# Performance work log

Hardware: AMD Instinct MI355X
Metric: run time of the kernel (lower is better)

## Reference

```python
import jax, jax.numpy as jnp
import numpy as np

MODEL_D = 512
N_HEADS = 8
D_K = 64
D_V = 64
EPS = 1e-5


def _layer_norm(x, g, b):
    mu = jnp.mean(x, axis=-1, keepdims=True)
    var = jnp.mean((x - mu) ** 2, axis=-1, keepdims=True)
    return (x - mu) * jax.lax.rsqrt(var + EPS) * g + b


def setup_inputs() -> dict:
    key = jax.random.key(0)
    ks = jax.random.split(key, 8)
    B, S = 8, 1024
    smiles = jax.random.normal(ks[0], (B, S, MODEL_D), dtype=jnp.float32)
    # causal mask: True where attention is disallowed (masked_fill semantics)
    mask = jnp.broadcast_to(jnp.triu(jnp.ones((S, S), dtype=bool), k=1), (B, S, S))
    sd = 1.0 / np.sqrt(MODEL_D)
    w_q = jax.random.normal(ks[1], (MODEL_D, N_HEADS * D_K), dtype=jnp.float32) * sd
    w_k = jax.random.normal(ks[2], (MODEL_D, N_HEADS * D_K), dtype=jnp.float32) * sd
    w_v = jax.random.normal(ks[3], (MODEL_D, N_HEADS * D_V), dtype=jnp.float32) * sd
    w_o = jax.random.normal(ks[4], (N_HEADS * D_V, MODEL_D), dtype=jnp.float32) * sd
    w1 = jax.random.normal(ks[5], (MODEL_D, 4 * MODEL_D), dtype=jnp.float32) * sd
    w2 = jax.random.normal(ks[6], (4 * MODEL_D, MODEL_D), dtype=jnp.float32) * (1.0 / np.sqrt(4 * MODEL_D))
    ln1_g = jnp.ones((MODEL_D,), jnp.float32)
    ln1_b = jnp.zeros((MODEL_D,), jnp.float32)
    ln2_g = jnp.ones((MODEL_D,), jnp.float32)
    ln2_b = jnp.zeros((MODEL_D,), jnp.float32)
    return {"smiles": smiles, "mask": mask, "w_q": w_q, "w_k": w_k, "w_v": w_v,
            "w_o": w_o, "ln1_g": ln1_g, "ln1_b": ln1_b, "w1": w1, "w2": w2,
            "ln2_g": ln2_g, "ln2_b": ln2_b}


def reference(smiles, mask, w_q, w_k, w_v, w_o, ln1_g, ln1_b, w1, w2, ln2_g, ln2_b):
    B, S, _ = smiles.shape
    # QKV projections -> [B, H, S, d]
    q = (smiles @ w_q).reshape(B, S, N_HEADS, D_K).transpose(0, 2, 1, 3)
    k = (smiles @ w_k).reshape(B, S, N_HEADS, D_K).transpose(0, 2, 1, 3)
    v = (smiles @ w_v).reshape(B, S, N_HEADS, D_V).transpose(0, 2, 1, 3)
    scores = jnp.einsum("bhqd,bhkd->bhqk", q, k) / np.sqrt(D_K)
    scores = jnp.where(mask[:, None, :, :], jnp.float32(-1e9), scores)
    attention = jax.nn.softmax(scores, axis=-1)
    ctx = jnp.einsum("bhqk,bhkd->bhqd", attention, v)
    ctx = ctx.transpose(0, 2, 1, 3).reshape(B, S, N_HEADS * D_V)
    attn_out = _layer_norm(ctx @ w_o + smiles, ln1_g, ln1_b)
    ffn = jax.nn.relu(attn_out @ w1) @ w2
    out = _layer_norm(ffn + attn_out, ln2_g, ln2_b)
    return out, attention
```

## Files before the change

kernel.cpp:

```cpp
#include <hip/hip_runtime.h>
#include <math.h>

#define BATCH 8
#define SEQ   1024
#define DMODEL 512
#define NHEADS 8
#define DKV   64
#define DFF   2048
#define ROWS  (BATCH * SEQ)
#define QKLD  1536

typedef __attribute__((ext_vector_type(8))) short short8;
typedef __attribute__((ext_vector_type(4))) float f32x4;

__device__ __forceinline__ short f2bf(float f) {
    unsigned u = __float_as_uint(f);
    u += 0x7FFFu + ((u >> 16) & 1u);
    return (short)(u >> 16);
}
__device__ __forceinline__ float bf2f(short s) {
    return __uint_as_float(((unsigned)(unsigned short)s) << 16);
}

#define GLD16(g, l) __builtin_amdgcn_global_load_lds( \
    (const __attribute__((address_space(1))) void*)(g), \
    (__attribute__((address_space(3))) void*)(l), 16, 0, 0)

__device__ __forceinline__ void stage128x32(const short* __restrict__ g, int ld,
                                            short* lds, int tid) {
    const int w = tid >> 6;
#pragma unroll
    for (int i = 0; i < 2; ++i) {
        const int L = i * 256 + tid;
        const int r = L >> 2, c = (L & 3) << 3;
        GLD16(g + (size_t)r * ld + c, lds + (size_t)(i * 256 + (w << 6)) * 8);
    }
}

template<int OUT_BF16, int RELU>
__global__ __launch_bounds__(256) void gemm_bt(const short* __restrict__ A,
                                               const short* __restrict__ Bt,
                                               void* __restrict__ Cv,
                                               int K, int lda, int ldb, int ldc,
                                               int qcols) {
    __shared__ short As[2][128 * 32];
    __shared__ short Bs[2][128 * 32];
    const int tid = threadIdx.x;

    const int nx = gridDim.x;
    const int nwg = nx * gridDim.y;
    const int flat = blockIdx.y * nx + blockIdx.x;
    const int swz = (flat & 7) * (nwg >> 3) + (flat >> 3);
    const int m0 = (swz / nx) * 128, n0 = (swz % nx) * 128;

    const int w = tid >> 6, lane = tid & 63;
    const int wr = (w >> 1) * 64, wc = (w & 1) * 64;
    const int lrow = lane & 15, hi = lane >> 4;

    f32x4 acc[4][4];
#pragma unroll
    for (int m = 0; m < 4; ++m)
#pragma unroll
        for (int n = 0; n < 4; ++n) acc[m][n] = {0.f, 0.f, 0.f, 0.f};

    const short* Ab = A + (size_t)m0 * lda;
    const short* Bb = Bt + (size_t)n0 * ldb;
    const int nt = K >> 5;

    stage128x32(Ab, lda, As[0], tid);
    stage128x32(Bb, ldb, Bs[0], tid);
    __syncthreads();

    int cur = 0;
    for (int t = 0; t < nt; ++t) {
        if (t + 1 < nt) {
            stage128x32(Ab + (size_t)(t + 1) * 32, lda, As[cur ^ 1], tid);
            stage128x32(Bb + (size_t)(t + 1) * 32, ldb, Bs[cur ^ 1], tid);
        }

        short8 af[4], bfr[4];
#pragma unroll
        for (int m = 0; m < 4; ++m)
            af[m] = *(const short8*)&As[cur][(size_t)(wr + m * 16 + lrow) * 32 + hi * 8];
#pragma unroll
        for (int n = 0; n < 4; ++n)
            bfr[n] = *(const short8*)&Bs[cur][(size_t)(wc + n * 16 + lrow) * 32 + hi * 8];
#pragma unroll
        for (int m = 0; m < 4; ++m)
#pragma unroll
            for (int n = 0; n < 4; ++n)
                acc[m][n] = __builtin_amdgcn_mfma_f32_16x16x32_bf16(bfr[n], af[m], acc[m][n], 0, 0, 0);

        __syncthreads();
        cur ^= 1;
    }

    const int orow = m0 + wr + lrow;
    const int ocol0 = n0 + wc + hi * 4;
#pragma unroll
    for (int m = 0; m < 4; ++m)
#pragma unroll
        for (int n = 0; n < 4; ++n) {
            const int col = ocol0 + n * 16;
            const float cs = (col < qcols) ? 0.125f : 1.0f;
            float v0 = acc[m][n][0], v1 = acc[m][n][1], v2 = acc[m][n][2], v3 = acc[m][n][3];
            if (RELU) {
                v0 = fmaxf(v0, 0.f); v1 = fmaxf(v1, 0.f);
                v2 = fmaxf(v2, 0.f); v3 = fmaxf(v3, 0.f);
            }
            v0 *= cs; v1 *= cs; v2 *= cs; v3 *= cs;
            const size_t off = (size_t)(orow + m * 16) * ldc + col;
            if (OUT_BF16) {
                short4 st = { f2bf(v0), f2bf(v1), f2bf(v2), f2bf(v3) };
                *(short4*)((short*)Cv + off) = st;
            } else {
                float4 st = { v0, v1, v2, v3 };
                *(float4*)((float*)Cv + off) = st;
            }
        }
}

__global__ __launch_bounds__(256, 2) void fused_attn(const short* __restrict__ Q,
                                                     const short* __restrict__ K,
                                                     const short* __restrict__ Vt,
                                                     float* __restrict__ attnP,
                                                     short* __restrict__ ctx) {
    const int flat = blockIdx.y * 8 + blockIdx.x;
    const int swz  = (flat & 7) * 64 + (flat >> 3);
    const int bh = swz >> 3, it = 7 - (swz & 7);
    const int b = bh >> 3, h = bh & 7;

    __shared__ short Qs[128 * 64];
    __shared__ short KVs[2][128 * 64];
    __shared__ short Ps[128 * 128];
    float* rsum = (float*)Ps;

    const int tid = threadIdx.x;
    const int w = tid >> 6, lane = tid & 63;
    const int wr = (w >> 1) * 64, wc2 = (w & 1);
    const int lrow = lane & 15, hi = lane >> 4;
    const size_t base = (size_t)b * SEQ * QKLD + h * DKV;
    float* aprow = attnP + (size_t)bh * SEQ * SEQ;

    auto stage_k = [&](int kt, short* dst) {
#pragma unroll
        for (int i = 0; i < 4; ++i) {
            const int L = i * 256 + tid;
            const int r = L >> 3, sc = ((L & 7) ^ (r & 7)) * 8;
            GLD16(K + base + (size_t)(kt * 128 + r) * QKLD + sc,
                  dst + (size_t)(i * 256 + (w << 6)) * 8);
        }
    };
    auto stage_v = [&](int kt, short* dst) {
#pragma unroll
        for (int i = 0; i < 4; ++i) {
            const int L = i * 256 + tid;
            const int r = L >> 4, sc = ((L & 15) ^ (r & 7)) * 8;
            GLD16(Vt + (size_t)(bh * DKV + r) * SEQ + kt * 128 + sc,
                  dst + (size_t)(i * 256 + (w << 6)) * 8);
        }
    };
    auto qkt = [&](const short* Ks, f32x4 s[4][4]) {
#pragma unroll
        for (int m = 0; m < 4; ++m)
#pragma unroll
            for (int n = 0; n < 4; ++n) s[m][n] = {0.f, 0.f, 0.f, 0.f};
#pragma unroll
        for (int sk = 0; sk < 2; ++sk) {
            short8 qf[4], kf[4];
#pragma unroll
            for (int m = 0; m < 4; ++m) {
                const int r = wr + m * 16 + lrow;
                qf[m] = *(const short8*)((const char*)Qs + r * 128 + ((hi * 16 + sk * 64) ^ ((r & 7) << 4)));
            }
#pragma unroll
            for (int n = 0; n < 4; ++n) {
                const int r = wc2 * 64 + n * 16 + lrow;
                kf[n] = *(const short8*)((const char*)Ks + r * 128 + ((hi * 16 + sk * 64) ^ ((r & 7) << 4)));
            }
#pragma unroll
            for (int m = 0; m < 4; ++m)
#pragma unroll
                for (int n = 0; n < 4; ++n)
                    s[m][n] = __builtin_amdgcn_mfma_f32_16x16x32_bf16(kf[n], qf[m], s[m][n], 0, 0, 0);
        }
    };

    {
        const int nz4 = (7 - it) * 32;
        if (nz4 > 0) {
            for (int r = tid >> 5; r < 128; r += 8) {
                float4* rp = (float4*)(aprow + (size_t)(it * 128 + r) * SEQ + (it + 1) * 128);
                for (int c = tid & 31; c < nz4; c += 32)
                    rp[c] = make_float4(0.f, 0.f, 0.f, 0.f);
            }
        }
    }

#pragma unroll
    for (int i = 0; i < 4; ++i) {
        const int L = i * 256 + tid;
        const int r = L >> 3, sc = ((L & 7) ^ (r & 7)) * 8;
        GLD16(Q + base + (size_t)(it * 128 + r) * QKLD + sc,
              Qs + (size_t)(i * 256 + (w << 6)) * 8);
    }
    stage_k(0, KVs[0]);
    stage_v(0, KVs[1]);
    __syncthreads();

    float rs[4] = {0.f, 0.f, 0.f, 0.f};
    f32x4 o[4][2];
#pragma unroll
    for (int m = 0; m < 4; ++m)
#pragma unroll
        for (int n = 0; n < 2; ++n) o[m][n] = {0.f, 0.f, 0.f, 0.f};

    for (int kt = 0; kt <= it; ++kt) {
        f32x4 s[4][4];
        qkt(KVs[0], s);

        const bool diag = (kt == it);
#pragma unroll
        for (int m = 0; m < 4; ++m) {
            const int q = wr + m * 16 + lrow;
#pragma unroll
            for (int n = 0; n < 4; ++n) {
                const int k0 = wc2 * 64 + n * 16 + hi * 4;
                float p0 = __expf(s[m][n][0]);
                float p1 = __expf(s[m][n][1]);
                float p2 = __expf(s[m][n][2]);
                float p3 = __expf(s[m][n][3]);
                if (diag) {
                    if (k0 + 0 > q) p0 = 0.f;
                    if (k0 + 1 > q) p1 = 0.f;
                    if (k0 + 2 > q) p2 = 0.f;
                    if (k0 + 3 > q) p3 = 0.f;
                }
                rs[m] += (p0 + p1) + (p2 + p3);
                short4 ph = { f2bf(p0), f2bf(p1), f2bf(p2), f2bf(p3) };
                *(short4*)((char*)Ps + q * 256 + ((k0 * 2) ^ ((q & 7) << 4))) = ph;
            }
        }
        __syncthreads();
        if (kt < it) stage_k(kt + 1, KVs[0]);

#pragma unroll
        for (int sk = 0; sk < 4; ++sk) {
            short8 pf[4], vf[2];
#pragma unroll
            for (int m = 0; m < 4; ++m) {
                const int r = wr + m * 16 + lrow;
                pf[m] = *(const short8*)((const char*)Ps + r * 256 + ((hi * 16 + sk * 64) ^ ((r & 7) << 4)));
            }
#pragma unroll
            for (int n = 0; n < 2; ++n) {
                const int r = wc2 * 32 + n * 16 + lrow;
                vf[n] = *(const short8*)((const char*)KVs[1] + r * 256 + ((hi * 16 + sk * 64) ^ ((r & 7) << 4)));
            }
#pragma unroll
            for (int m = 0; m < 4; ++m)
#pragma unroll
                for (int n = 0; n < 2; ++n)
                    o[m][n] = __builtin_amdgcn_mfma_f32_16x16x32_bf16(vf[n], pf[m], o[m][n], 0, 0, 0);
        }
        __syncthreads();
        if (kt < it) stage_v(kt + 1, KVs[1]);
    }

#pragma unroll
    for (int m = 0; m < 4; ++m) {
        rs[m] += __shfl_xor(rs[m], 16);
        rs[m] += __shfl_xor(rs[m], 32);
    }
    if (lane < 16) {
#pragma unroll
        for (int m = 0; m < 4; ++m)
            rsum[wc2 * 128 + wr + m * 16 + lane] = rs[m];
    }
    __syncthreads();
    if (tid < 128) rsum[tid] = 1.0f / (rsum[tid] + rsum[128 + tid]);
    __syncthreads();
    float inv[4];
#pragma unroll
    for (int m = 0; m < 4; ++m) inv[m] = rsum[wr + m * 16 + lrow];

#pragma unroll
    for (int m = 0; m < 4; ++m) {
        const int q = it * 128 + wr + m * 16 + lrow;
#pragma unroll
        for (int n = 0; n < 2; ++n) {
            const int d = h * DKV + wc2 * 32 + n * 16 + hi * 4;
            short4 st = { f2bf(o[m][n][0] * inv[m]), f2bf(o[m][n][1] * inv[m]),
                          f2bf(o[m][n][2] * inv[m]), f2bf(o[m][n][3] * inv[m]) };
            *(short4*)(ctx + (size_t)(b * SEQ + q) * DMODEL + d) = st;
        }
    }

    stage_k(0, KVs[0]);
    __syncthreads();
    int cur = 0;
    for (int kt = 0; kt <= it; ++kt) {
        if (kt < it) stage_k(kt + 1, KVs[cur ^ 1]);

        f32x4 s[4][4];
        qkt(KVs[cur], s);

        const bool diag = (kt == it);
#pragma unroll
        for (int m = 0; m < 4; ++m) {
            const int q = wr + m * 16 + lrow;
#pragma unroll
            for (int n = 0; n < 4; ++n) {
                const int k0 = wc2 * 64 + n * 16 + hi * 4;
                float p0 = __expf(s[m][n][0]);
                float p1 = __expf(s[m][n][1]);
                float p2 = __expf(s[m][n][2]);
                float p3 = __expf(s[m][n][3]);
                if (diag) {
                    if (k0 + 0 > q) p0 = 0.f;
                    if (k0 + 1 > q) p1 = 0.f;
                    if (k0 + 2 > q) p2 = 0.f;
                    if (k0 + 3 > q) p3 = 0.f;
                }
                float4 pv4 = { p0 * inv[m], p1 * inv[m], p2 * inv[m], p3 * inv[m] };
                *(float4*)(aprow + (size_t)(it * 128 + q) * SEQ + kt * 128 + k0) = pv4;
            }
        }
        __syncthreads();
        cur ^= 1;
    }
}

template<int RES_BF16, int OUT_F32, int OUT_BF16>
__global__ __launch_bounds__(128) void residual_ln(const float* __restrict__ xin,
                                                   const void* __restrict__ res,
                                                   const float* __restrict__ g,
                                                   const float* __restrict__ beta,
                                                   float* __restrict__ outf,
                                                   short* __restrict__ outh) {
    const int row = blockIdx.x;
    const int tid = threadIdx.x;

    float4 v = ((const float4*)(xin + (size_t)row * DMODEL))[tid];
    if (RES_BF16) {
        const short4 rr = ((const short4*)((const short*)res + (size_t)row * DMODEL))[tid];
        v.x += bf2f(rr.x); v.y += bf2f(rr.y); v.z += bf2f(rr.z); v.w += bf2f(rr.w);
    } else {
        const float4 rr = ((const float4*)((const float*)res + (size_t)row * DMODEL))[tid];
        v.x += rr.x; v.y += rr.y; v.z += rr.z; v.w += rr.w;
    }

    float sum = v.x + v.y + v.z + v.w;
    float sq  = v.x * v.x + v.y * v.y + v.z * v.z + v.w * v.w;
#pragma unroll
    for (int off = 32; off > 0; off >>= 1) {
        sum += __shfl_down(sum, off);
        sq  += __shfl_down(sq, off);
    }
    __shared__ float s_sum[2], s_sq[2];
    const int wid = tid >> 6, lane = tid & 63;
    if (lane == 0) { s_sum[wid] = sum; s_sq[wid] = sq; }
    __syncthreads();

    const float tsum = s_sum[0] + s_sum[1];
    const float tsq  = s_sq[0] + s_sq[1];
    const float mu   = tsum * (1.0f / DMODEL);
    const float var  = tsq * (1.0f / DMODEL) - mu * mu;
    const float rstd = rsqrtf(var + 1e-5f);

    const float4 gg = ((const float4*)g)[tid];
    const float4 bb = ((const float4*)beta)[tid];
    float4 o;
    o.x = (v.x - mu) * rstd * gg.x + bb.x;
    o.y = (v.y - mu) * rstd * gg.y + bb.y;
    o.z = (v.z - mu) * rstd * gg.z + bb.z;
    o.w = (v.w - mu) * rstd * gg.w + bb.w;
    if (OUT_F32) ((float4*)(outf + (size_t)row * DMODEL))[tid] = o;
    if (OUT_BF16) {
        short4 oh = { f2bf(o.x), f2bf(o.y), f2bf(o.z), f2bf(o.w) };
        ((short4*)(outh + (size_t)row * DMODEL))[tid] = oh;
    }
}

__global__ __launch_bounds__(256) void convert_bf16(const float* __restrict__ X,
                                                    short* __restrict__ Xh) {
    const size_t i = (size_t)blockIdx.x * 256 + threadIdx.x;
    const float4* p = (const float4*)X + i * 2;
    const float4 a = p[0], b = p[1];
    short8 o = { f2bf(a.x), f2bf(a.y), f2bf(a.z), f2bf(a.w),
                 f2bf(b.x), f2bf(b.y), f2bf(b.z), f2bf(b.w) };
    *(short8*)(Xh + i * 8) = o;
}

__global__ __launch_bounds__(256) void transpose_w(const float* __restrict__ W,
                                                   short* __restrict__ Wt,
                                                   int K, int N) {
    __shared__ float t[32][33];
    const int n0 = blockIdx.x * 32, k0 = blockIdx.y * 32;
    const int tx = threadIdx.x, ty = threadIdx.y;
#pragma unroll
    for (int i = 0; i < 4; ++i)
        t[ty + i * 8][tx] = W[(size_t)(k0 + ty + i * 8) * N + n0 + tx];
    __syncthreads();
#pragma unroll
    for (int i = 0; i < 4; ++i)
        Wt[(size_t)(n0 + ty + i * 8) * K + k0 + tx] = f2bf(t[tx][ty + i * 8]);
}

__global__ __launch_bounds__(256) void transpose_v(const short* __restrict__ QKV,
                                                   short* __restrict__ Vt) {
    __shared__ short t[32][33];
    const int s0 = blockIdx.x * 32, d0 = blockIdx.y * 32, bh = blockIdx.z;
    const int b = bh >> 3, h = bh & 7;
    const int tx = threadIdx.x, ty = threadIdx.y;
#pragma unroll
    for (int i = 0; i < 4; ++i)
        t[ty + i * 8][tx] = QKV[(size_t)(b * SEQ + s0 + ty + i * 8) * QKLD + 1024 + h * DKV + d0 + tx];
    __syncthreads();
#pragma unroll
    for (int i = 0; i < 4; ++i)
        Vt[(size_t)(bh * DKV + d0 + ty + i * 8) * SEQ + s0 + tx] = t[tx][ty + i * 8];
}

extern "C" void kernel_launch(void* const* d_in, const int* in_sizes, int n_in,
                              void* d_out, int out_size, void* d_ws, size_t ws_size,
                              hipStream_t stream) {
    const float* X    = (const float*)d_in[0];
    const float* w_q  = (const float*)d_in[2];
    const float* w_k  = (const float*)d_in[3];
    const float* w_v  = (const float*)d_in[4];
    const float* w_o  = (const float*)d_in[5];
    const float* ln1g = (const float*)d_in[6];
    const float* ln1b = (const float*)d_in[7];
    const float* w1   = (const float*)d_in[8];
    const float* w2   = (const float*)d_in[9];
    const float* ln2g = (const float*)d_in[10];
    const float* ln2b = (const float*)d_in[11];

    float* out   = (float*)d_out;
    float* attnP = out + (size_t)ROWS * DMODEL;

    const size_t M = 1u << 20;
    short* ws    = (short*)d_ws;
    short* qkv   = ws;
    short* Vt    = ws + 12 * M;
    short* ctxh  = ws + 16 * M;
    short* aoutH = ws + 20 * M;
    short* Xh    = ws + 24 * M;
    short* wqkvt = ws + 28 * M;
    short* wot   = wqkvt + 786432;
    short* w1t   = ws + 29 * M;
    short* w2t   = ws + 30 * M;
    short* hbuf  = ws;

    convert_bf16<<<dim3(2048), dim3(256), 0, stream>>>(X, Xh);
    transpose_w<<<dim3(16, 16), dim3(32, 8), 0, stream>>>(w_q, wqkvt, DMODEL, DMODEL);
    transpose_w<<<dim3(16, 16), dim3(32, 8), 0, stream>>>(w_k, wqkvt + 512 * 512, DMODEL, DMODEL);
    transpose_w<<<dim3(16, 16), dim3(32, 8), 0, stream>>>(w_v, wqkvt + 1024 * 512, DMODEL, DMODEL);
    transpose_w<<<dim3(16, 16), dim3(32, 8), 0, stream>>>(w_o, wot, DMODEL, DMODEL);
    transpose_w<<<dim3(64, 16), dim3(32, 8), 0, stream>>>(w1, w1t, DMODEL, DFF);
    transpose_w<<<dim3(16, 64), dim3(32, 8), 0, stream>>>(w2, w2t, DFF, DMODEL);

    gemm_bt<1, 0><<<dim3(12, 64), dim3(256), 0, stream>>>(Xh, wqkvt, qkv,
                                                          DMODEL, DMODEL, DMODEL, QKLD, 512);
    transpose_v<<<dim3(32, 2, 64), dim3(32, 8), 0, stream>>>(qkv, Vt);

    fused_attn<<<dim3(8, 64), dim3(256), 0, stream>>>(qkv, qkv + 512, Vt, attnP, ctxh);

    gemm_bt<0, 0><<<dim3(4, 64), dim3(256), 0, stream>>>(ctxh, wot, out,
                                                         DMODEL, DMODEL, DMODEL, DMODEL, 0);
    residual_ln<0, 0, 1><<<dim3(ROWS), dim3(128), 0, stream>>>(out, X, ln1g, ln1b, nullptr, aoutH);

    gemm_bt<1, 1><<<dim3(16, 64), dim3(256), 0, stream>>>(aoutH, w1t, hbuf,
                                                          DMODEL, DMODEL, DMODEL, DFF, 0);
    gemm_bt<0, 0><<<dim3(4, 64), dim3(256), 0, stream>>>(hbuf, w2t, out,
                                                         DFF, DFF, DFF, DMODEL, 0);
    residual_ln<1, 1, 0><<<dim3(ROWS), dim3(128), 0, stream>>>(out, aoutH, ln2g, ln2b, out, nullptr);
}
```

Measured before the change: 234.9 us.

## Defer attention-probability writes into FFN1 kernel and merge weight-prep launches

The attention kernel no longer recomputes QK^T to write the full probability matrix. It now stores the per-row inverse softmax sums to a small buffer. A new combined kernel interleaves FFN1 GEMM blocks with blocks that recompute scores and write the normalized probabilities and causal zeros, so the write-bandwidth-heavy output overlaps with compute-bound GEMM work. The input conversion and the six weight-transpose launches are also merged into one prep kernel, and workspace offsets are reshuffled to fit the new buffers. The cost is that the combined kernel uses a larger shared-memory footprint for all its blocks, and its heterogeneous blocks may balance unevenly.

```diff
diff --git a/kernel.cpp b/kernel.cpp
--- a/kernel.cpp
+++ b/kernel.cpp
@@ -34,6 +34,45 @@
         const int L = i * 256 + tid;
         const int r = L >> 2, c = (L & 3) << 3;
         GLD16(g + (size_t)r * ld + c, lds + (size_t)(i * 256 + (w << 6)) * 8);
+    }
+}
+
+__device__ __forceinline__ void stage_k128(const short* __restrict__ Kp, size_t base,
+                                           int kt, short* dst, int tid, int w) {
+#pragma unroll
+    for (int i = 0; i < 4; ++i) {
+        const int L = i * 256 + tid;
+        const int r = L >> 3, sc = ((L & 7) ^ (r & 7)) * 8;
+        GLD16(Kp + base + (size_t)(kt * 128 + r) * QKLD + sc,
+              dst + (size_t)(i * 256 + (w << 6)) * 8);
+    }
+}
+
+__device__ __forceinline__ void qkt_body(const short* Qs, const short* Ks,
+                                         int wr, int wc2, int lrow, int hi,
+                                         f32x4 s[4][4]) {
+#pragma unroll
+    for (int m = 0; m < 4; ++m)
+#pragma unroll
+        for (int n = 0; n < 4; ++n) s[m][n] = {0.f, 0.f, 0.f, 0.f};
+#pragma unroll
+    for (int sk = 0; sk < 2; ++sk) {
+        short8 qf[4], kf[4];
+#pragma unroll
+        for (int m = 0; m < 4; ++m) {
+            const int r = wr + m * 16 + lrow;
+            qf[m] = *(const short8*)((const char*)Qs + r * 128 + ((hi * 16 + sk * 64) ^ ((r & 7) << 4)));
+        }
+#pragma unroll
+        for (int n = 0; n < 4; ++n) {
+            const int r = wc2 * 64 + n * 16 + lrow;
+            kf[n] = *(const short8*)((const char*)Ks + r * 128 + ((hi * 16 + sk * 64) ^ ((r & 7) << 4)));
+        }
+#pragma unroll
+        for (int m = 0; m < 4; ++m)
+#pragma unroll
+            for (int n = 0; n < 4; ++n)
+                s[m][n] = __builtin_amdgcn_mfma_f32_16x16x32_bf16(kf[n], qf[m], s[m][n], 0, 0, 0);
     }
 }
 
@@ -77,7 +116,6 @@
             stage128x32(Ab + (size_t)(t + 1) * 32, lda, As[cur ^ 1], tid);
             stage128x32(Bb + (size_t)(t + 1) * 32, ldb, Bs[cur ^ 1], tid);
         }
-
         short8 af[4], bfr[4];
 #pragma unroll
         for (int m = 0; m < 4; ++m)
@@ -90,7 +128,6 @@
 #pragma unroll
             for (int n = 0; n < 4; ++n)
                 acc[m][n] = __builtin_amdgcn_mfma_f32_16x16x32_bf16(bfr[n], af[m], acc[m][n], 0, 0, 0);
-
         __syncthreads();
         cur ^= 1;
     }
@@ -120,11 +157,11 @@
         }
 }
 
-__global__ __launch_bounds__(256, 2) void fused_attn(const short* __restrict__ Q,
-                                                     const short* __restrict__ K,
-                                                     const short* __restrict__ Vt,
-                                                     float* __restrict__ attnP,
-                                                     short* __restrict__ ctx) {
+__global__ __launch_bounds__(256, 2) void attn_ctx(const short* __restrict__ Q,
+                                                   const short* __restrict__ K,
+                                                   const short* __restrict__ Vt,
+                                                   short* __restrict__ ctx,
+                                                   float* __restrict__ invg) {
     const int flat = blockIdx.y * 8 + blockIdx.x;
     const int swz  = (flat & 7) * 64 + (flat >> 3);
     const int bh = swz >> 3, it = 7 - (swz & 7);
@@ -140,17 +177,7 @@
     const int wr = (w >> 1) * 64, wc2 = (w & 1);
     const int lrow = lane & 15, hi = lane >> 4;
     const size_t base = (size_t)b * SEQ * QKLD + h * DKV;
-    float* aprow = attnP + (size_t)bh * SEQ * SEQ;
-
-    auto stage_k = [&](int kt, short* dst) {
-#pragma unroll
-        for (int i = 0; i < 4; ++i) {
-            const int L = i * 256 + tid;
-            const int r = L >> 3, sc = ((L & 7) ^ (r & 7)) * 8;
-            GLD16(K + base + (size_t)(kt * 128 + r) * QKLD + sc,
-                  dst + (size_t)(i * 256 + (w << 6)) * 8);
-        }
-    };
+
     auto stage_v = [&](int kt, short* dst) {
 #pragma unroll
         for (int i = 0; i < 4; ++i) {
@@ -160,42 +187,6 @@
                   dst + (size_t)(i * 256 + (w << 6)) * 8);
         }
     };
-    auto qkt = [&](const short* Ks, f32x4 s[4][4]) {
-#pragma unroll
-        for (int m = 0; m < 4; ++m)
-#pragma unroll
-            for (int n = 0; n < 4; ++n) s[m][n] = {0.f, 0.f, 0.f, 0.f};
-#pragma unroll
-        for (int sk = 0; sk < 2; ++sk) {
-            short8 qf[4], kf[4];
-#pragma unroll
-            for (int m = 0; m < 4; ++m) {
-                const int r = wr + m * 16 + lrow;
-                qf[m] = *(const short8*)((const char*)Qs + r * 128 + ((hi * 16 + sk * 64) ^ ((r & 7) << 4)));
-            }
-#pragma unroll
-            for (int n = 0; n < 4; ++n) {
-                const int r = wc2 * 64 + n * 16 + lrow;
-                kf[n] = *(const short8*)((const char*)Ks + r * 128 + ((hi * 16 + sk * 64) ^ ((r & 7) << 4)));
-            }
-#pragma unroll
-            for (int m = 0; m < 4; ++m)
-#pragma unroll
-                for (int n = 0; n < 4; ++n)
-                    s[m][n] = __builtin_amdgcn_mfma_f32_16x16x32_bf16(kf[n], qf[m], s[m][n], 0, 0, 0);
-        }
-    };
-
-    {
-        const int nz4 = (7 - it) * 32;
-        if (nz4 > 0) {
-            for (int r = tid >> 5; r < 128; r += 8) {
-                float4* rp = (float4*)(aprow + (size_t)(it * 128 + r) * SEQ + (it + 1) * 128);
-                for (int c = tid & 31; c < nz4; c += 32)
-                    rp[c] = make_float4(0.f, 0.f, 0.f, 0.f);
-            }
-        }
-    }
 
 #pragma unroll
     for (int i = 0; i < 4; ++i) {
@@ -204,7 +195,7 @@
         GLD16(Q + base + (size_t)(it * 128 + r) * QKLD + sc,
               Qs + (size_t)(i * 256 + (w << 6)) * 8);
     }
-    stage_k(0, KVs[0]);
+    stage_k128(K, base, 0, KVs[0], tid, w);
     stage_v(0, KVs[1]);
     __syncthreads();
 
@@ -217,7 +208,7 @@
 
     for (int kt = 0; kt <= it; ++kt) {
         f32x4 s[4][4];
-        qkt(KVs[0], s);
+        qkt_body(Qs, KVs[0], wr, wc2, lrow, hi, s);
 
         const bool diag = (kt == it);
 #pragma unroll
@@ -242,7 +233,7 @@
             }
         }
         __syncthreads();
-        if (kt < it) stage_k(kt + 1, KVs[0]);
+        if (kt < it) stage_k128(K, base, kt + 1, KVs[0], tid, w);
 
 #pragma unroll
         for (int sk = 0; sk < 4; ++sk) {
@@ -278,7 +269,11 @@
             rsum[wc2 * 128 + wr + m * 16 + lane] = rs[m];
     }
     __syncthreads();
-    if (tid < 128) rsum[tid] = 1.0f / (rsum[tid] + rsum[128 + tid]);
+    if (tid < 128) {
+        const float iv = 1.0f / (rsum[tid] + rsum[128 + tid]);
+        rsum[tid] = iv;
+        invg[(size_t)bh * SEQ + it * 128 + tid] = iv;
+    }
     __syncthreads();
     float inv[4];
 #pragma unroll
@@ -295,39 +290,148 @@
             *(short4*)(ctx + (size_t)(b * SEQ + q) * DMODEL + d) = st;
         }
     }
-
-    stage_k(0, KVs[0]);
-    __syncthreads();
-    int cur = 0;
-    for (int kt = 0; kt <= it; ++kt) {
-        if (kt < it) stage_k(kt + 1, KVs[cur ^ 1]);
-
-        f32x4 s[4][4];
-        qkt(KVs[cur], s);
-
-        const bool diag = (kt == it);
-#pragma unroll
-        for (int m = 0; m < 4; ++m) {
-            const int q = wr + m * 16 + lrow;
+}
+
+__global__ __launch_bounds__(256) void ffn1_pwrite(const short* __restrict__ Am,
+                                                   const short* __restrict__ w1t,
+                                                   short* __restrict__ hbuf,
+                                                   const short* __restrict__ Q,
+                                                   const short* __restrict__ K,
+                                                   const float* __restrict__ invg,
+                                                   float* __restrict__ attnP) {
+    __shared__ short smem[24576];
+    const int tid = threadIdx.x;
+    const int w = tid >> 6, lane = tid & 63;
+    const int lrow = lane & 15, hi = lane >> 4;
+    const int flat = blockIdx.x;
+
+    if (flat % 3 != 0) {
+        const int f = flat - flat / 3 - 1;
+        const int swz = (f & 7) * 128 + (f >> 3);
+        const int m0 = (swz >> 4) * 128, n0 = (swz & 15) * 128;
+        const int wr = (w >> 1) * 64, wc = (w & 1) * 64;
+
+        short* As0 = smem;
+        short* As1 = smem + 4096;
+        short* Bs0 = smem + 8192;
+        short* Bs1 = smem + 12288;
+
+        f32x4 acc[4][4];
+#pragma unroll
+        for (int m = 0; m < 4; ++m)
+#pragma unroll
+            for (int n = 0; n < 4; ++n) acc[m][n] = {0.f, 0.f, 0.f, 0.f};
+
+        const short* Ab = Am + (size_t)m0 * DMODEL;
+        const short* Bb = w1t + (size_t)n0 * DMODEL;
+
+        stage128x32(Ab, DMODEL, As0, tid);
+        stage128x32(Bb, DMODEL, Bs0, tid);
+        __syncthreads();
+
+        for (int t = 0; t < 16; ++t) {
+            short* Ac = (t & 1) ? As1 : As0;
+            short* Bc = (t & 1) ? Bs1 : Bs0;
+            if (t + 1 < 16) {
+                short* An = (t & 1) ? As0 : As1;
+                short* Bn = (t & 1) ? Bs0 : Bs1;
+                stage128x32(Ab + (size_t)(t + 1) * 32, DMODEL, An, tid);
+                stage128x32(Bb + (size_t)(t + 1) * 32, DMODEL, Bn, tid);
+            }
+            short8 af[4], bfr[4];
+#pragma unroll
+            for (int m = 0; m < 4; ++m)
+                af[m] = *(const short8*)&Ac[(size_t)(wr + m * 16 + lrow) * 32 + hi * 8];
+#pragma unroll
+            for (int n = 0; n < 4; ++n)
+                bfr[n] = *(const short8*)&Bc[(size_t)(wc + n * 16 + lrow) * 32 + hi * 8];
+#pragma unroll
+            for (int m = 0; m < 4; ++m)
+#pragma unroll
+                for (int n = 0; n < 4; ++n)
+                    acc[m][n] = __builtin_amdgcn_mfma_f32_16x16x32_bf16(bfr[n], af[m], acc[m][n], 0, 0, 0);
+            __syncthreads();
+        }
+
+        const int orow = m0 + wr + lrow;
+        const int ocol0 = n0 + wc + hi * 4;
+#pragma unroll
+        for (int m = 0; m < 4; ++m)
 #pragma unroll
             for (int n = 0; n < 4; ++n) {
-                const int k0 = wc2 * 64 + n * 16 + hi * 4;
-                float p0 = __expf(s[m][n][0]);
-                float p1 = __expf(s[m][n][1]);
-                float p2 = __expf(s[m][n][2]);
-                float p3 = __expf(s[m][n][3]);
-                if (diag) {
-                    if (k0 + 0 > q) p0 = 0.f;
-                    if (k0 + 1 > q) p1 = 0.f;
-                    if (k0 + 2 > q) p2 = 0.f;
-                    if (k0 + 3 > q) p3 = 0.f;
+                short4 st = { f2bf(fmaxf(acc[m][n][0], 0.f)), f2bf(fmaxf(acc[m][n][1], 0.f)),
+                              f2bf(fmaxf(acc[m][n][2], 0.f)), f2bf(fmaxf(acc[m][n][3], 0.f)) };
+                *(short4*)(hbuf + (size_t)(orow + m * 16) * DFF + ocol0 + n * 16) = st;
+            }
+    } else {
+        const int p = flat / 3;
+        const int swz = (p & 7) * 64 + (p >> 3);
+        const int bh = swz >> 3, it = 7 - (swz & 7);
+        const int b = bh >> 3, h = bh & 7;
+        const int wr = (w >> 1) * 64, wc2 = (w & 1);
+        const size_t base = (size_t)b * SEQ * QKLD + h * DKV;
+        float* aprow = attnP + (size_t)bh * SEQ * SEQ;
+
+        short* Qs  = smem;
+        short* Ks0 = smem + 8192;
+        short* Ks1 = smem + 16384;
+
+        {
+            const int nz4 = (7 - it) * 32;
+            if (nz4 > 0) {
+                for (int r = tid >> 5; r < 128; r += 8) {
+                    float4* rp = (float4*)(aprow + (size_t)(it * 128 + r) * SEQ + (it + 1) * 128);
+                    for (int c = tid & 31; c < nz4; c += 32)
+                        rp[c] = make_float4(0.f, 0.f, 0.f, 0.f);
                 }
-                float4 pv4 = { p0 * inv[m], p1 * inv[m], p2 * inv[m], p3 * inv[m] };
-                *(float4*)(aprow + (size_t)(it * 128 + q) * SEQ + kt * 128 + k0) = pv4;
-            }
-        }
+            }
+        }
+
+#pragma unroll
+        for (int i = 0; i < 4; ++i) {
+            const int L = i * 256 + tid;
+            const int r = L >> 3, sc = ((L & 7) ^ (r & 7)) * 8;
+            GLD16(Q + base + (size_t)(it * 128 + r) * QKLD + sc,
+                  Qs + (size_t)(i * 256 + (w << 6)) * 8);
+        }
+        stage_k128(K, base, 0, Ks0, tid, w);
+
+        float inv[4];
+#pragma unroll
+        for (int m = 0; m < 4; ++m)
+            inv[m] = invg[(size_t)bh * SEQ + it * 128 + wr + m * 16 + lrow];
         __syncthreads();
-        cur ^= 1;
+
+        for (int kt = 0; kt <= it; ++kt) {
+            short* Kc = (kt & 1) ? Ks1 : Ks0;
+            if (kt < it) stage_k128(K, base, kt + 1, (kt & 1) ? Ks0 : Ks1, tid, w);
+
+            f32x4 s[4][4];
+            qkt_body(Qs, Kc, wr, wc2, lrow, hi, s);
+
+            const bool diag = (kt == it);
+#pragma unroll
+            for (int m = 0; m < 4; ++m) {
+                const int q = wr + m * 16 + lrow;
+#pragma unroll
+                for (int n = 0; n < 4; ++n) {
+                    const int k0 = wc2 * 64 + n * 16 + hi * 4;
+                    float p0 = __expf(s[m][n][0]);
+                    float p1 = __expf(s[m][n][1]);
+                    float p2 = __expf(s[m][n][2]);
+                    float p3 = __expf(s[m][n][3]);
+                    if (diag) {
+                        if (k0 + 0 > q) p0 = 0.f;
+                        if (k0 + 1 > q) p1 = 0.f;
+                        if (k0 + 2 > q) p2 = 0.f;
+                        if (k0 + 3 > q) p3 = 0.f;
+                    }
+                    float4 pv4 = { p0 * inv[m], p1 * inv[m], p2 * inv[m], p3 * inv[m] };
+                    *(float4*)(aprow + (size_t)(it * 128 + q) * SEQ + kt * 128 + k0) = pv4;
+                }
+            }
+            __syncthreads();
+        }
     }
 }
 
@@ -382,29 +486,51 @@
     }
 }
 
-__global__ __launch_bounds__(256) void convert_bf16(const float* __restrict__ X,
-                                                    short* __restrict__ Xh) {
-    const size_t i = (size_t)blockIdx.x * 256 + threadIdx.x;
-    const float4* p = (const float4*)X + i * 2;
-    const float4 a = p[0], b = p[1];
-    short8 o = { f2bf(a.x), f2bf(a.y), f2bf(a.z), f2bf(a.w),
-                 f2bf(b.x), f2bf(b.y), f2bf(b.z), f2bf(b.w) };
-    *(short8*)(Xh + i * 8) = o;
-}
-
-__global__ __launch_bounds__(256) void transpose_w(const float* __restrict__ W,
-                                                   short* __restrict__ Wt,
-                                                   int K, int N) {
-    __shared__ float t[32][33];
-    const int n0 = blockIdx.x * 32, k0 = blockIdx.y * 32;
-    const int tx = threadIdx.x, ty = threadIdx.y;
+__global__ __launch_bounds__(256) void prep_all(const float* __restrict__ X,
+                                                const float* __restrict__ w_q,
+                                                const float* __restrict__ w_k,
+                                                const float* __restrict__ w_v,
+                                                const float* __restrict__ w_o,
+                                                const float* __restrict__ w1,
+                                                const float* __restrict__ w2,
+                                                short* __restrict__ Xh,
+                                                short* __restrict__ wqkvt,
+                                                short* __restrict__ wot,
+                                                short* __restrict__ w1t,
+                                                short* __restrict__ w2t) {
+    const int flat = blockIdx.x;
+    const int tid = threadIdx.x;
+    if (flat < 2048) {
+        const size_t i = (size_t)flat * 256 + tid;
+        const float4* p = (const float4*)X + i * 2;
+        const float4 a = p[0], b = p[1];
+        short8 o = { f2bf(a.x), f2bf(a.y), f2bf(a.z), f2bf(a.w),
+                     f2bf(b.x), f2bf(b.y), f2bf(b.z), f2bf(b.w) };
+        *(short8*)(Xh + i * 8) = o;
+        return;
+    }
+    const int t = flat - 2048;
+    const float* W; short* Wt; int K, N, tile;
+    if (t < 1024) {
+        const int wsel = t >> 8; tile = t & 255;
+        K = 512; N = 512;
+        W  = (wsel == 0) ? w_q : (wsel == 1) ? w_k : (wsel == 2) ? w_v : w_o;
+        Wt = (wsel < 3) ? (wqkvt + (size_t)wsel * 512 * 512) : wot;
+    } else if (t < 2048) { tile = t - 1024; K = 512;  N = 2048; W = w1; Wt = w1t; }
+    else                 { tile = t - 2048; K = 2048; N = 512;  W = w2; Wt = w2t; }
+
+    const int ntx = N >> 5;
+    const int n0 = (tile % ntx) * 32, k0 = (tile / ntx) * 32;
+    const int tx = tid & 31, ty = tid >> 5;
+
+    __shared__ float tb[32][33];
 #pragma unroll
     for (int i = 0; i < 4; ++i)
-        t[ty + i * 8][tx] = W[(size_t)(k0 + ty + i * 8) * N + n0 + tx];
+        tb[ty + i * 8][tx] = W[(size_t)(k0 + ty + i * 8) * N + n0 + tx];
     __syncthreads();
 #pragma unroll
     for (int i = 0; i < 4; ++i)
-        Wt[(size_t)(n0 + ty + i * 8) * K + k0 + tx] = f2bf(t[tx][ty + i * 8]);
+        Wt[(size_t)(n0 + ty + i * 8) * K + k0 + tx] = f2bf(tb[tx][ty + i * 8]);
 }
 
 __global__ __launch_bounds__(256) void transpose_v(const short* __restrict__ QKV,
@@ -444,35 +570,32 @@
     short* ws    = (short*)d_ws;
     short* qkv   = ws;
     short* Vt    = ws + 12 * M;
-    short* ctxh  = ws + 16 * M;
-    short* aoutH = ws + 20 * M;
+    short* ctxh  = ws + 28 * M;
+    short* aoutH = ws + 16 * M;
     short* Xh    = ws + 24 * M;
-    short* wqkvt = ws + 28 * M;
+    short* wqkvt = ws + 20 * M;
     short* wot   = wqkvt + 786432;
-    short* w1t   = ws + 29 * M;
-    short* w2t   = ws + 30 * M;
-    short* hbuf  = ws;
-
-    convert_bf16<<<dim3(2048), dim3(256), 0, stream>>>(X, Xh);
-    transpose_w<<<dim3(16, 16), dim3(32, 8), 0, stream>>>(w_q, wqkvt, DMODEL, DMODEL);
-    transpose_w<<<dim3(16, 16), dim3(32, 8), 0, stream>>>(w_k, wqkvt + 512 * 512, DMODEL, DMODEL);
-    transpose_w<<<dim3(16, 16), dim3(32, 8), 0, stream>>>(w_v, wqkvt + 1024 * 512, DMODEL, DMODEL);
-    transpose_w<<<dim3(16, 16), dim3(32, 8), 0, stream>>>(w_o, wot, DMODEL, DMODEL);
-    transpose_w<<<dim3(64, 16), dim3(32, 8), 0, stream>>>(w1, w1t, DMODEL, DFF);
-    transpose_w<<<dim3(16, 64), dim3(32, 8), 0, stream>>>(w2, w2t, DFF, DMODEL);
+    short* w1t   = ws + 21 * M;
+    short* w2t   = ws + 22 * M;
+    float* invg  = (float*)(ws + 23 * M);
+    short* hbuf  = ws + 24 * M;
+
+    prep_all<<<dim3(5120), dim3(256), 0, stream>>>(X, w_q, w_k, w_v, w_o, w1, w2,
+                                                   Xh, wqkvt, wot, w1t, w2t);
 
     gemm_bt<1, 0><<<dim3(12, 64), dim3(256), 0, stream>>>(Xh, wqkvt, qkv,
                                                           DMODEL, DMODEL, DMODEL, QKLD, 512);
     transpose_v<<<dim3(32, 2, 64), dim3(32, 8), 0, stream>>>(qkv, Vt);
 
-    fused_attn<<<dim3(8, 64), dim3(256), 0, stream>>>(qkv, qkv + 512, Vt, attnP, ctxh);
+    attn_ctx<<<dim3(8, 64), dim3(256), 0, stream>>>(qkv, qkv + 512, Vt, ctxh, invg);
 
     gemm_bt<0, 0><<<dim3(4, 64), dim3(256), 0, stream>>>(ctxh, wot, out,
                                                          DMODEL, DMODEL, DMODEL, DMODEL, 0);
     residual_ln<0, 0, 1><<<dim3(ROWS), dim3(128), 0, stream>>>(out, X, ln1g, ln1b, nullptr, aoutH);
 
-    gemm_bt<1, 1><<<dim3(16, 64), dim3(256), 0, stream>>>(aoutH, w1t, hbuf,
-                                                          DMODEL, DMODEL, DMODEL, DFF, 0);
+    ffn1_pwrite<<<dim3(1536), dim3(256), 0, stream>>>(aoutH, w1t, hbuf,
+                                                      qkv, qkv + 512, invg, attnP);
+
     gemm_bt<0, 0><<<dim3(4, 64), dim3(256), 0, stream>>>(hbuf, w2t, out,
                                                          DFF, DFF, DFF, DMODEL, 0);
     residual_ln<1, 1, 0><<<dim3(ROWS), dim3(128), 0, stream>>>(out, aoutH, ln2g, ln2b, out, nullptr);
```

New measurement: 238.6 us. About the same (+1.6%).
